# Kernel optimization log

Hardware: AMD Instinct MI355X
Metric: run time of the kernel (lower is better)

## Reference

```python
import jax, jax.numpy as jnp
import numpy as np

N_HIDDEN = 15


def lstm_cell(x, h, c, W_ih, W_hh, b_ih, b_hh):
    # x: [B, in], h/c: [B, H]. PyTorch LSTMCell gate order: i, f, g, o
    gates = x @ W_ih.T + h @ W_hh.T + b_ih + b_hh  # [B, 4H]
    i, f, g, o = jnp.split(gates, 4, axis=-1)
    i = jax.nn.sigmoid(i)
    f = jax.nn.sigmoid(f)
    g = jnp.tanh(g)
    o = jax.nn.sigmoid(o)
    c_new = f * c + i * g
    h_new = o * jnp.tanh(c_new)
    return h_new, c_new


def setup_inputs() -> dict:
    key = jax.random.key(0)
    ks = jax.random.split(key, 12)
    B, T, H = 4096, 1024, N_HIDDEN
    s = 1.0 / np.sqrt(H)  # torch default init bound
    u = lambda k, shape: jax.random.uniform(k, shape, jnp.float32, -s, s)
    return {
        "input": jax.random.normal(ks[0], (B, T), jnp.float32),
        "W_ih1": u(ks[1], (4 * H, 1)),
        "W_hh1": u(ks[2], (4 * H, H)),
        "b_ih1": u(ks[3], (4 * H,)),
        "b_hh1": u(ks[4], (4 * H,)),
        "W_ih2": u(ks[5], (4 * H, H)),
        "W_hh2": u(ks[6], (4 * H, H)),
        "b_ih2": u(ks[7], (4 * H,)),
        "b_hh2": u(ks[8], (4 * H,)),
        "W_lin": u(ks[9], (1, H)),
        "b_lin": u(ks[10], (1,)),
        "future": 64,
    }


def reference(input, W_ih1, W_hh1, b_ih1, b_hh1, W_ih2, W_hh2, b_ih2, b_hh2, W_lin, b_lin, future):
    B = input.shape[0]
    H = N_HIDDEN
    zeros = jnp.zeros((B, H), input.dtype)

    def step(carry, x_t):
        h1, c1, h2, c2 = carry
        h1, c1 = lstm_cell(x_t, h1, c1, W_ih1, W_hh1, b_ih1, b_hh1)
        h2, c2 = lstm_cell(h1, h2, c2, W_ih2, W_hh2, b_ih2, b_hh2)
        out = h2 @ W_lin.T + b_lin  # [B, 1]
        return (h1, c1, h2, c2), out

    xs = input.T[:, :, None]  # [T, B, 1]
    carry, outs = jax.lax.scan(step, (zeros, zeros, zeros, zeros), xs)

    last_out = outs[-1]  # [B, 1]

    def fut_step(carry, _):
        h1, c1, h2, c2, out = carry
        (h1, c1, h2, c2), out = step((h1, c1, h2, c2), out)
        return (h1, c1, h2, c2, out), out

    _, fut_outs = jax.lax.scan(fut_step, (*carry, last_out), None, length=future)

    all_outs = jnp.concatenate([outs, fut_outs], axis=0)  # [T+future, B, 1]
    return all_outs[:, :, 0].T  # [B, T+future]
```

## Files before the change

### kernel.cpp

```cpp
#include <hip/hip_runtime.h>

#define HID   15
#define TMAIN 1024
#define FUT   64
#define OUTW  (TMAIN + FUT)

typedef _Float16 v2h __attribute__((ext_vector_type(2)));

__device__ __forceinline__ float rcp_(float x)  { return __builtin_amdgcn_rcpf(x); }
__device__ __forceinline__ float exp2_(float x) { return __builtin_amdgcn_exp2f(x); }
__device__ __forceinline__ float tanh_(float x) {
    return __builtin_fmaf(2.0f, rcp_(1.0f + exp2_(x * -2.885390081777927f)), -1.0f);
}

template<int I> struct ic { static constexpr int v = I; };
template<int J, int N, class F>
__device__ __forceinline__ void unroll_for(F&& f) {
    if constexpr (J < N) { f(ic<J>{}); unroll_for<J + 1, N>(f); }
}

template<int CTRL>
__device__ __forceinline__ int dppi(int x) {
    return __builtin_amdgcn_update_dpp(0, x, CTRL, 0xF, 0xF, true);
}
template<int CTRL>
__device__ __forceinline__ float dppf(float x) {
    return __int_as_float(dppi<CTRL>(__float_as_int(x)));
}
__device__ __forceinline__ float row_sum_bcast(float p) {
    p += dppf<0x111>(p);
    p += dppf<0x112>(p);
    p += dppf<0x114>(p);
    p += dppf<0x118>(p);
    return dppf<0x15F>(p);
}
__device__ __forceinline__ float fdot2(v2h a, v2h b, float c) {
    return __builtin_amdgcn_fdot2(a, b, c, false);
}
__device__ __forceinline__ v2h pkrtz(float lo, float hi) {
    return __builtin_bit_cast(v2h, __builtin_amdgcn_cvt_pkrtz(lo, hi));
}

__global__ __launch_bounds__(256)
__attribute__((amdgpu_waves_per_eu(1, 1)))
void lstm_seq_kernel(const float* __restrict__ input,
                     const float* __restrict__ W_ih1, const float* __restrict__ W_hh1,
                     const float* __restrict__ b_ih1, const float* __restrict__ b_hh1,
                     const float* __restrict__ W_ih2, const float* __restrict__ W_hh2,
                     const float* __restrict__ b_ih2, const float* __restrict__ b_hh2,
                     const float* __restrict__ W_lin, const float* __restrict__ b_lin,
                     float* __restrict__ out)
{
    const int tid  = threadIdx.x;
    const int wq   = tid >> 6;
    const int lane = tid & 63;
    const int g    = lane >> 4;
    const int k    = lane & 15;
    const int b0   = (blockIdx.x * 4 + wq) * 4;

    const bool pad = (k >= HID);
    const float m  = pad ? 0.0f : 1.0f;
    const int  kk  = pad ? 0 : k;

    const float L2E = 1.442695040888963f;
    const float sA[4] = {-L2E, -L2E, -2.0f * L2E, -L2E};

    v2h w1[4][8], w2i[4][8], w2h[4][8];
    float bb1[4], bb2[4];
    #pragma unroll
    for (int gi = 0; gi < 4; ++gi) {
        const int row = gi * HID + kk;
        const float s = m * sA[gi];
        bb1[gi] = s * (b_ih1[row] + b_hh1[row]);
        bb2[gi] = s * (b_ih2[row] + b_hh2[row]);
        #pragma unroll
        for (int j = 0; j < 8; ++j) {
            const int c0 = 2 * j, c1i = 2 * j + 1;
            w1 [gi][j] = (v2h){(_Float16)(s * W_hh1[row * HID + c0]),
                               (_Float16)((c1i < HID) ? s * W_hh1[row * HID + c1i]
                                                      : s * W_ih1[row])};
            w2i[gi][j] = (v2h){(_Float16)(s * W_ih2[row * HID + c0]),
                               (_Float16)((c1i < HID) ? s * W_ih2[row * HID + c1i] : 0.0f)};
            w2h[gi][j] = (v2h){(_Float16)(s * W_hh2[row * HID + c0]),
                               (_Float16)((c1i < HID) ? s * W_hh2[row * HID + c1i] : 0.0f)};
        }
    }
    const float wl   = m * W_lin[kk];
    const float blin = b_lin[0];

    auto packh = [&](float h) -> int {
        const _Float16 hh = (_Float16)h;
        const int lo = (int)(unsigned short)__builtin_bit_cast(unsigned short, hh);
        const int hi = dppi<0x101>(lo);
        const v2h pr = {__builtin_bit_cast(_Float16, (unsigned short)lo),
                        __builtin_bit_cast(_Float16, (unsigned short)(hi & 0xFFFF))};
        return __builtin_bit_cast(int, pr);
    };

    v2h hb1[8];
    #pragma unroll
    for (int j = 0; j < 8; ++j) hb1[j] = (v2h){(_Float16)0.0f, (_Float16)0.0f};
    int hpk2 = 0;
    float c1 = 0.0f, c2 = 0.0f, outv = 0.0f;

    auto step = [&](auto Sc, auto UseOvC, float xvpre, float& oreg) {
        constexpr int  S      = decltype(Sc)::v;
        constexpr bool USE_OV = decltype(UseOvC)::v;

        float a0 = bb1[0], a1 = bb1[1], a2 = bb1[2], a3 = bb1[3];
        unroll_for<0, 8>([&](auto jc) {
            constexpr int j = decltype(jc)::v;
            a0 = fdot2(w1[0][j], hb1[j], a0);
            a1 = fdot2(w1[1][j], hb1[j], a1);
            a2 = fdot2(w1[2][j], hb1[j], a2);
            a3 = fdot2(w1[3][j], hb1[j], a3);
        });

        float d0 = bb2[0], d1 = bb2[1], d2 = bb2[2], d3 = bb2[3];
        unroll_for<0, 8>([&](auto jc) {
            constexpr int j = decltype(jc)::v;
            const v2h hb = __builtin_bit_cast(v2h, dppi<0x150 + 2*j>(hpk2));
            d0 = fdot2(w2h[0][j], hb, d0);
            d1 = fdot2(w2h[1][j], hb, d1);
            d2 = fdot2(w2h[2][j], hb, d2);
            d3 = fdot2(w2h[3][j], hb, d3);
        });

        const float ig = rcp_(1.0f + exp2_(a0));
        const float fg = rcp_(1.0f + exp2_(a1));
        const float gg = __builtin_fmaf(2.0f, rcp_(1.0f + exp2_(a2)), -1.0f);
        const float og = rcp_(1.0f + exp2_(a3));
        c1 = __builtin_fmaf(fg, c1, ig * gg);
        const float h1n = og * tanh_(c1);

        const int hpk1 = packh(h1n);
        unroll_for<0, 8>([&](auto jc) {
            constexpr int j = decltype(jc)::v;
            hb1[j] = __builtin_bit_cast(v2h, dppi<0x150 + 2*j>(hpk1));
        });
        unroll_for<0, 8>([&](auto jc) {
            constexpr int j = decltype(jc)::v;
            d0 = fdot2(w2i[0][j], hb1[j], d0);
            d1 = fdot2(w2i[1][j], hb1[j], d1);
            d2 = fdot2(w2i[2][j], hb1[j], d2);
            d3 = fdot2(w2i[3][j], hb1[j], d3);
        });

        const float i2 = rcp_(1.0f + exp2_(d0));
        const float f2 = rcp_(1.0f + exp2_(d1));
        const float g2 = __builtin_fmaf(2.0f, rcp_(1.0f + exp2_(d2)), -1.0f);
        const float o2 = rcp_(1.0f + exp2_(d3));
        c2 = __builtin_fmaf(f2, c2, i2 * g2);
        const float h2n = o2 * tanh_(c2);
        hpk2 = packh(h2n);

        const float ov = row_sum_bcast(wl * h2n) + blin;
        oreg = (k == S) ? ov : oreg;

        const float xv = USE_OV ? ov : xvpre;
        hb1[7] = pkrtz(dppf<0x15E>(h1n), xv);

        outv = ov;
    };

    const size_t inb  = (size_t)(b0 + g) * TMAIN + k;
    const size_t outb = (size_t)(b0 + g) * OUTW  + k;

    float xcur = input[inb];
    hb1[7] = pkrtz(0.0f, dppf<0x150>(xcur));

    #pragma unroll 1
    for (int ch = 0; ch < TMAIN / 16; ++ch) {
        const bool last = (ch == TMAIN / 16 - 1);
        const float xnext = input[inb + (last ? ch : ch + 1) * 16];
        float oreg = 0.0f;
        unroll_for<0, 16>([&](auto sc) {
            constexpr int s = decltype(sc)::v;
            if constexpr (s < 15) {
                step(sc, ic<0>{}, dppf<0x150 + s + 1>(xcur), oreg);
            } else {
                if (last) step(sc, ic<1>{}, 0.0f, oreg);
                else      step(sc, ic<0>{}, dppf<0x150>(xnext), oreg);
            }
        });
        out[outb + ch * 16] = oreg;
        xcur = xnext;
    }

    #pragma unroll 1
    for (int ch = 0; ch < FUT / 16; ++ch) {
        float oreg = 0.0f;
        unroll_for<0, 16>([&](auto sc) {
            step(sc, ic<1>{}, 0.0f, oreg);
        });
        out[outb + TMAIN + ch * 16] = oreg;
    }
}

extern "C" void kernel_launch(void* const* d_in, const int* in_sizes, int n_in,
                              void* d_out, int out_size, void* d_ws, size_t ws_size,
                              hipStream_t stream)
{
    const float* input = (const float*)d_in[0];
    const float* W_ih1 = (const float*)d_in[1];
    const float* W_hh1 = (const float*)d_in[2];
    const float* b_ih1 = (const float*)d_in[3];
    const float* b_hh1 = (const float*)d_in[4];
    const float* W_ih2 = (const float*)d_in[5];
    const float* W_hh2 = (const float*)d_in[6];
    const float* b_ih2 = (const float*)d_in[7];
    const float* b_hh2 = (const float*)d_in[8];
    const float* W_lin = (const float*)d_in[9];
    const float* b_lin = (const float*)d_in[10];

    lstm_seq_kernel<<<256, 256, 0, stream>>>(
        input, W_ih1, W_hh1, b_ih1, b_hh1,
        W_ih2, W_hh2, b_ih2, b_hh2, W_lin, b_lin,
        (float*)d_out);
}
```

Measured before the change: 473.0 us.

## Compute LSTM gate matvecs with 16x16x32 fp16 MFMA instead of fdot2 chains

Replaces the per-lane fdot2 dot-product chains for both LSTM layers with four MFMA 16x16x32 f16 instructions per layer per step. Weights are packed into A-fragments, and the hidden state is gathered into the B-fragment via ds_bpermute and ds_swizzle rather than DPP. The output reduction now uses swizzles plus a bpermute, and input and output are chunked by 8 instead of 16. The aim is to shorten the serial per-step dependency chain by using matrix cores. In exchange it adds MFMA latency, LDS-crossbar permute latency and select logic on every recurrent step.

```diff
diff --git a/kernel.cpp b/kernel.cpp
--- a/kernel.cpp
+++ b/kernel.cpp
@@ -5,7 +5,10 @@
 #define FUT   64
 #define OUTW  (TMAIN + FUT)
 
-typedef _Float16 v2h __attribute__((ext_vector_type(2)));
+typedef _Float16 v2h   __attribute__((ext_vector_type(2)));
+typedef _Float16 v8h   __attribute__((ext_vector_type(8)));
+typedef float    f32x4 __attribute__((ext_vector_type(4)));
+typedef int      i32x4 __attribute__((ext_vector_type(4)));
 
 __device__ __forceinline__ float rcp_(float x)  { return __builtin_amdgcn_rcpf(x); }
 __device__ __forceinline__ float exp2_(float x) { return __builtin_amdgcn_exp2f(x); }
@@ -19,26 +22,19 @@
     if constexpr (J < N) { f(ic<J>{}); unroll_for<J + 1, N>(f); }
 }
 
-template<int CTRL>
-__device__ __forceinline__ int dppi(int x) {
-    return __builtin_amdgcn_update_dpp(0, x, CTRL, 0xF, 0xF, true);
-}
-template<int CTRL>
-__device__ __forceinline__ float dppf(float x) {
-    return __int_as_float(dppi<CTRL>(__float_as_int(x)));
-}
-__device__ __forceinline__ float row_sum_bcast(float p) {
-    p += dppf<0x111>(p);
-    p += dppf<0x112>(p);
-    p += dppf<0x114>(p);
-    p += dppf<0x118>(p);
-    return dppf<0x15F>(p);
-}
-__device__ __forceinline__ float fdot2(v2h a, v2h b, float c) {
-    return __builtin_amdgcn_fdot2(a, b, c, false);
-}
+template<int PAT>
+__device__ __forceinline__ int swzi(int x) { return __builtin_amdgcn_ds_swizzle(x, PAT); }
+template<int PAT>
+__device__ __forceinline__ float swzf(float x) { return __int_as_float(swzi<PAT>(__float_as_int(x))); }
+
+__device__ __forceinline__ int bpermi(int addr, int x) { return __builtin_amdgcn_ds_bpermute(addr, x); }
+__device__ __forceinline__ float bpermf(int addr, float x) { return __int_as_float(bpermi(addr, __float_as_int(x))); }
+
 __device__ __forceinline__ v2h pkrtz(float lo, float hi) {
     return __builtin_bit_cast(v2h, __builtin_amdgcn_cvt_pkrtz(lo, hi));
+}
+__device__ __forceinline__ f32x4 mfma16(v8h a, v8h b, f32x4 c) {
+    return __builtin_amdgcn_mfma_f32_16x16x32_f16(a, b, c, 0, 0, 0);
 }
 
 __global__ __launch_bounds__(256)
@@ -54,146 +50,186 @@
     const int tid  = threadIdx.x;
     const int wq   = tid >> 6;
     const int lane = tid & 63;
-    const int g    = lane >> 4;
-    const int k    = lane & 15;
+    const int u    = lane >> 4;
+    const int c    = lane & 15;
+    const int s    = c & 3;
+    const int cg   = c >> 2;
     const int b0   = (blockIdx.x * 4 + wq) * 4;
-
-    const bool pad = (k >= HID);
-    const float m  = pad ? 0.0f : 1.0f;
-    const int  kk  = pad ? 0 : k;
 
     const float L2E = 1.442695040888963f;
     const float sA[4] = {-L2E, -L2E, -2.0f * L2E, -L2E};
 
-    v2h w1[4][8], w2i[4][8], w2h[4][8];
-    float bb1[4], bb2[4];
+    v8h   A1[4], A2[4];
+    f32x4 C1[4], C2[4];
     #pragma unroll
-    for (int gi = 0; gi < 4; ++gi) {
-        const int row = gi * HID + kk;
-        const float s = m * sA[gi];
-        bb1[gi] = s * (b_ih1[row] + b_hh1[row]);
-        bb2[gi] = s * (b_ih2[row] + b_hh2[row]);
+    for (int m = 0; m < 4; ++m) {
         #pragma unroll
-        for (int j = 0; j < 8; ++j) {
-            const int c0 = 2 * j, c1i = 2 * j + 1;
-            w1 [gi][j] = (v2h){(_Float16)(s * W_hh1[row * HID + c0]),
-                               (_Float16)((c1i < HID) ? s * W_hh1[row * HID + c1i]
-                                                      : s * W_ih1[row])};
-            w2i[gi][j] = (v2h){(_Float16)(s * W_ih2[row * HID + c0]),
-                               (_Float16)((c1i < HID) ? s * W_ih2[row * HID + c1i] : 0.0f)};
-            w2h[gi][j] = (v2h){(_Float16)(s * W_hh2[row * HID + c0]),
-                               (_Float16)((c1i < HID) ? s * W_hh2[row * HID + c1i] : 0.0f)};
-        }
-    }
-    const float wl   = m * W_lin[kk];
+        for (int e = 0; e < 8; ++e) {
+            const int k    = (e < 4) ? (4 * u + e) : (16 + 4 * u + (e - 4));
+            const int gate = c & 3;
+            const int U    = 4 * m + (c >> 2);
+            float v1 = 0.0f, v2 = 0.0f;
+            if (U < HID) {
+                const int wr = gate * HID + U;
+                if (k < HID)            v1 = W_hh1[wr * HID + k];
+                else if (k == HID)      v1 = W_ih1[wr];
+                if (k < HID)            v2 = W_ih2[wr * HID + k];
+                else if (k >= 16 && k < 16 + HID) v2 = W_hh2[wr * HID + (k - 16)];
+            }
+            A1[m][e] = (_Float16)(sA[gate] * v1);
+            A2[m][e] = (_Float16)(sA[gate] * v2);
+        }
+        #pragma unroll
+        for (int r = 0; r < 4; ++r) {
+            const int U = 4 * m + u;
+            float bv1 = 0.0f, bv2 = 0.0f;
+            if (U < HID) {
+                const int wr = r * HID + U;
+                bv1 = sA[r] * (b_ih1[wr] + b_hh1[wr]);
+                bv2 = sA[r] * (b_ih2[wr] + b_hh2[wr]);
+            }
+            C1[m][r] = bv1; C2[m][r] = bv2;
+        }
+    }
+
+    const int   Uh   = 4 * cg + u;
+    const float wl2  = (Uh < HID) ? W_lin[Uh] : 0.0f;
     const float blin = b_lin[0];
 
-    auto packh = [&](float h) -> int {
-        const _Float16 hh = (_Float16)h;
-        const int lo = (int)(unsigned short)__builtin_bit_cast(unsigned short, hh);
-        const int hi = dppi<0x101>(lo);
-        const v2h pr = {__builtin_bit_cast(_Float16, (unsigned short)lo),
-                        __builtin_bit_cast(_Float16, (unsigned short)(hi & 0xFFFF))};
-        return __builtin_bit_cast(int, pr);
+    int bpa[4];
+    #pragma unroll
+    for (int q = 0; q < 4; ++q) {
+        const int P    = 2 * u + (q & 1);
+        const int usrc = (q < 2) ? 2 * (P & 1) : 1 + 2 * (P & 1);
+        bpa[q] = (((usrc << 4) + 4 * (P >> 1) + s) << 2);
+    }
+    const int  a32    = (lane ^ 32) << 2;
+    const bool uodd   = (u & 1) != 0;
+    const bool cgb0   = (cg & 1) != 0;
+    const bool cgb1   = (cg & 2) != 0;
+    const bool xmask  = (u == 2) && (cg == 3);
+    const int  myslot = (lane >> 2) & 7;
+
+    int B0 = 0, B1 = 0, B2 = 0, B3 = 0;
+    int HP = 0;
+    float c1v = 0.0f, c2v = 0.0f;
+
+    auto rebuildB = [&]() {
+        B0 = bpermi(bpa[0], HP);
+        B1 = bpermi(bpa[1], HP);
+        B2 = bpermi(bpa[2], HP);
+        B3 = bpermi(bpa[3], HP);
     };
-
-    v2h hb1[8];
-    #pragma unroll
-    for (int j = 0; j < 8; ++j) hb1[j] = (v2h){(_Float16)0.0f, (_Float16)0.0f};
-    int hpk2 = 0;
-    float c1 = 0.0f, c2 = 0.0f, outv = 0.0f;
 
     auto step = [&](auto Sc, auto UseOvC, float xvpre, float& oreg) {
         constexpr int  S      = decltype(Sc)::v;
         constexpr bool USE_OV = decltype(UseOvC)::v;
 
-        float a0 = bb1[0], a1 = bb1[1], a2 = bb1[2], a3 = bb1[3];
-        unroll_for<0, 8>([&](auto jc) {
-            constexpr int j = decltype(jc)::v;
-            a0 = fdot2(w1[0][j], hb1[j], a0);
-            a1 = fdot2(w1[1][j], hb1[j], a1);
-            a2 = fdot2(w1[2][j], hb1[j], a2);
-            a3 = fdot2(w1[3][j], hb1[j], a3);
-        });
-
-        float d0 = bb2[0], d1 = bb2[1], d2 = bb2[2], d3 = bb2[3];
-        unroll_for<0, 8>([&](auto jc) {
-            constexpr int j = decltype(jc)::v;
-            const v2h hb = __builtin_bit_cast(v2h, dppi<0x150 + 2*j>(hpk2));
-            d0 = fdot2(w2h[0][j], hb, d0);
-            d1 = fdot2(w2h[1][j], hb, d1);
-            d2 = fdot2(w2h[2][j], hb, d2);
-            d3 = fdot2(w2h[3][j], hb, d3);
-        });
-
-        const float ig = rcp_(1.0f + exp2_(a0));
-        const float fg = rcp_(1.0f + exp2_(a1));
-        const float gg = __builtin_fmaf(2.0f, rcp_(1.0f + exp2_(a2)), -1.0f);
-        const float og = rcp_(1.0f + exp2_(a3));
-        c1 = __builtin_fmaf(fg, c1, ig * gg);
-        const float h1n = og * tanh_(c1);
-
-        const int hpk1 = packh(h1n);
-        unroll_for<0, 8>([&](auto jc) {
-            constexpr int j = decltype(jc)::v;
-            hb1[j] = __builtin_bit_cast(v2h, dppi<0x150 + 2*j>(hpk1));
-        });
-        unroll_for<0, 8>([&](auto jc) {
-            constexpr int j = decltype(jc)::v;
-            d0 = fdot2(w2i[0][j], hb1[j], d0);
-            d1 = fdot2(w2i[1][j], hb1[j], d1);
-            d2 = fdot2(w2i[2][j], hb1[j], d2);
-            d3 = fdot2(w2i[3][j], hb1[j], d3);
-        });
-
-        const float i2 = rcp_(1.0f + exp2_(d0));
-        const float f2 = rcp_(1.0f + exp2_(d1));
-        const float g2 = __builtin_fmaf(2.0f, rcp_(1.0f + exp2_(d2)), -1.0f);
-        const float o2 = rcp_(1.0f + exp2_(d3));
-        c2 = __builtin_fmaf(f2, c2, i2 * g2);
-        const float h2n = o2 * tanh_(c2);
-        hpk2 = packh(h2n);
-
-        const float ov = row_sum_bcast(wl * h2n) + blin;
-        oreg = (k == S) ? ov : oreg;
-
-        const float xv = USE_OV ? ov : xvpre;
-        hb1[7] = pkrtz(dppf<0x15E>(h1n), xv);
-
-        outv = ov;
+        const v8h Bv = __builtin_bit_cast(v8h, (i32x4){B0, B1, B2, B3});
+        f32x4 d0 = mfma16(A1[0], Bv, C1[0]);
+        f32x4 d1 = mfma16(A1[1], Bv, C1[1]);
+        f32x4 d2 = mfma16(A1[2], Bv, C1[2]);
+        f32x4 d3 = mfma16(A1[3], Bv, C1[3]);
+
+        float P0, P1, P2, P3;
+        {
+            float t0, t1;
+            t0 = cgb0 ? d1[0] : d0[0]; t1 = cgb0 ? d3[0] : d2[0]; P0 = cgb1 ? t1 : t0;
+            t0 = cgb0 ? d1[1] : d0[1]; t1 = cgb0 ? d3[1] : d2[1]; P1 = cgb1 ? t1 : t0;
+            t0 = cgb0 ? d1[2] : d0[2]; t1 = cgb0 ? d3[2] : d2[2]; P2 = cgb1 ? t1 : t0;
+            t0 = cgb0 ? d1[3] : d0[3]; t1 = cgb0 ? d3[3] : d2[3]; P3 = cgb1 ? t1 : t0;
+        }
+
+        const float ig = rcp_(1.0f + exp2_(P0));
+        const float fg = rcp_(1.0f + exp2_(P1));
+        const float gg = __builtin_fmaf(2.0f, rcp_(1.0f + exp2_(P2)), -1.0f);
+        const float og = rcp_(1.0f + exp2_(P3));
+        c1v = __builtin_fmaf(fg, c1v, ig * gg);
+        const float h1n = og * tanh_(c1v);
+
+        const float prt1 = swzf<0x401F>(h1n);
+        const float hi1  = xmask ? xvpre : prt1;
+        const int   h1p  = __builtin_bit_cast(int, pkrtz(h1n, hi1));
+        HP = uodd ? HP : h1p;
+        rebuildB();
+
+        const v8h Bv2 = __builtin_bit_cast(v8h, (i32x4){B0, B1, B2, B3});
+        f32x4 e0 = mfma16(A2[0], Bv2, C2[0]);
+        f32x4 e1 = mfma16(A2[1], Bv2, C2[1]);
+        f32x4 e2 = mfma16(A2[2], Bv2, C2[2]);
+        f32x4 e3 = mfma16(A2[3], Bv2, C2[3]);
+
+        float Q0, Q1, Q2, Q3;
+        {
+            float t0, t1;
+            t0 = cgb0 ? e1[0] : e0[0]; t1 = cgb0 ? e3[0] : e2[0]; Q0 = cgb1 ? t1 : t0;
+            t0 = cgb0 ? e1[1] : e0[1]; t1 = cgb0 ? e3[1] : e2[1]; Q1 = cgb1 ? t1 : t0;
+            t0 = cgb0 ? e1[2] : e0[2]; t1 = cgb0 ? e3[2] : e2[2]; Q2 = cgb1 ? t1 : t0;
+            t0 = cgb0 ? e1[3] : e0[3]; t1 = cgb0 ? e3[3] : e2[3]; Q3 = cgb1 ? t1 : t0;
+        }
+
+        const float i2 = rcp_(1.0f + exp2_(Q0));
+        const float f2 = rcp_(1.0f + exp2_(Q1));
+        const float g2 = __builtin_fmaf(2.0f, rcp_(1.0f + exp2_(Q2)), -1.0f);
+        const float o2 = rcp_(1.0f + exp2_(Q3));
+        c2v = __builtin_fmaf(f2, c2v, i2 * g2);
+        const float h2n = o2 * tanh_(c2v);
+
+        float pv = wl2 * h2n;
+        pv += swzf<0x101F>(pv);
+        pv += swzf<0x201F>(pv);
+        pv += swzf<0x401F>(pv);
+        pv += bpermf(a32, pv);
+        const float ov = pv + blin;
+        oreg = (myslot == S) ? ov : oreg;
+
+        const float prt2 = swzf<0x401F>(h2n);
+        const int   h2p  = __builtin_bit_cast(int, pkrtz(prt2, h2n));
+        HP = uodd ? h2p : HP;
+
+        if constexpr (USE_OV) {
+            const int hx = __builtin_bit_cast(int, pkrtz(h1n, ov));
+            HP = xmask ? hx : HP;
+            B1 = bpermi(bpa[1], HP);
+        }
     };
 
-    const size_t inb  = (size_t)(b0 + g) * TMAIN + k;
-    const size_t outb = (size_t)(b0 + g) * OUTW  + k;
+    const size_t inb  = (size_t)(b0 + s) * TMAIN + myslot;
+    const size_t outb = (size_t)(b0 + s) * OUTW  + myslot;
 
     float xcur = input[inb];
-    hb1[7] = pkrtz(0.0f, dppf<0x150>(xcur));
+    {
+        const float x0 = swzf<3>(xcur);
+        const int p1 = __builtin_bit_cast(int, pkrtz(0.0f, xmask ? x0 : 0.0f));
+        HP = uodd ? 0 : p1;
+        rebuildB();
+    }
 
     #pragma unroll 1
-    for (int ch = 0; ch < TMAIN / 16; ++ch) {
-        const bool last = (ch == TMAIN / 16 - 1);
-        const float xnext = input[inb + (last ? ch : ch + 1) * 16];
+    for (int ch = 0; ch < TMAIN / 8; ++ch) {
+        const bool last = (ch == TMAIN / 8 - 1);
+        const float xnext = input[inb + (size_t)(last ? ch : ch + 1) * 8];
         float oreg = 0.0f;
-        unroll_for<0, 16>([&](auto sc) {
-            constexpr int s = decltype(sc)::v;
-            if constexpr (s < 15) {
-                step(sc, ic<0>{}, dppf<0x150 + s + 1>(xcur), oreg);
+        unroll_for<0, 8>([&](auto sc) {
+            constexpr int sI = decltype(sc)::v;
+            if constexpr (sI < 7) {
+                step(sc, ic<0>{}, swzf<((sI + 1) * 128) | 3>(xcur), oreg);
             } else {
                 if (last) step(sc, ic<1>{}, 0.0f, oreg);
-                else      step(sc, ic<0>{}, dppf<0x150>(xnext), oreg);
+                else      step(sc, ic<0>{}, swzf<3>(xnext), oreg);
             }
         });
-        out[outb + ch * 16] = oreg;
+        if (lane < 32) out[outb + (size_t)ch * 8] = oreg;
         xcur = xnext;
     }
 
     #pragma unroll 1
-    for (int ch = 0; ch < FUT / 16; ++ch) {
+    for (int fc = 0; fc < FUT / 8; ++fc) {
         float oreg = 0.0f;
-        unroll_for<0, 16>([&](auto sc) {
+        unroll_for<0, 8>([&](auto sc) {
             step(sc, ic<1>{}, 0.0f, oreg);
         });
-        out[outb + TMAIN + ch * 16] = oreg;
+        if (lane < 32) out[outb + TMAIN + (size_t)fc * 8] = oreg;
     }
 }
 
```

New measurement: 529.0 us. 11.8% more time.
